# Kernel optimization log

Hardware: AMD Instinct MI355X
Metric: run time of the kernel (lower is better)

Reference implementation:

```python
import jax, jax.numpy as jnp
import numpy as np

B, SD, AD, H, QE, NQ = 16384, 512, 64, 1024, 64, 64


def setup_inputs() -> dict:
    key = jax.random.key(0)
    ks = jax.random.split(key, 12)
    s = 0.02
    p = lambda k, shape: (jax.random.normal(k, shape, jnp.float32) * s)
    return {
        "state": jax.random.normal(ks[0], (B, SD), jnp.float32),
        "action": jax.random.normal(ks[1], (B, AD), jnp.float32),
        # twin critics: leading axis 2 stacks q1 / q2 parameters
        "W_e1": p(ks[2], (2, QE, 1)),      "b_e1": p(ks[3], (2, QE)),
        "W_e2": p(ks[4], (2, QE, QE)),     "b_e2": p(ks[5], (2, QE)),
        "W_f1": p(ks[6], (2, H, SD + AD)), "b_f1": p(ks[7], (2, H)),
        "g1": jnp.ones((2, H), jnp.float32),  "beta1": jnp.zeros((2, H), jnp.float32),
        "W_f2": p(ks[8], (2, H, H)),       "b_f2": p(ks[9], (2, H)),
        "g2": jnp.ones((2, H), jnp.float32),  "beta2": jnp.zeros((2, H), jnp.float32),
        "W_h": p(ks[10], (2, 1, H + QE)),  "b_h": p(ks[11], (2, 1)),
    }


def _layernorm(x, g, b, eps=1e-5):
    mu = x.mean(-1, keepdims=True)
    var = ((x - mu) ** 2).mean(-1, keepdims=True)
    return (x - mu) * jax.lax.rsqrt(var + eps) * g + b


def _qnet(state, action, W_e1, b_e1, W_e2, b_e2, W_f1, b_f1, g1, beta1,
          W_f2, b_f2, g2, beta2, W_h, b_h):
    # feature_net (eval mode: dropout is identity)
    x = jnp.concatenate([state, action], axis=-1)            # [B, SD+AD]
    h = jax.nn.relu(_layernorm(x @ W_f1.T + b_f1, g1, beta1))
    feat = jax.nn.relu(_layernorm(h @ W_f2.T + b_f2, g2, beta2))  # [B, H]
    # tau embedding (batch-independent -> compute once per quantile, not per sample)
    tau = (jnp.linspace(0.0, 1.0, NQ + 1)[:-1] + 1.0 / (2 * NQ))[:, None]  # [NQ,1]
    te = jax.nn.relu(tau @ W_e1.T + b_e1) @ W_e2.T + b_e2    # [NQ, QE]
    # head on concat([feat, te]) == linear split (exact same math as the 64-iter loop)
    q_feat = feat @ W_h[0, :H]                               # [B]
    q_tau = te @ W_h[0, H:]                                  # [NQ]
    return q_feat[:, None] + q_tau[None, :] + b_h[0]         # [B, NQ]


def reference(state, action, W_e1, b_e1, W_e2, b_e2, W_f1, b_f1, g1, beta1,
              W_f2, b_f2, g2, beta2, W_h, b_h):
    qnet = lambda *ps: _qnet(state, action, *ps)
    q = jax.vmap(qnet)(W_e1, b_e1, W_e2, b_e2, W_f1, b_f1, g1, beta1,
                       W_f2, b_f2, g2, beta2, W_h, b_h)      # [2, B, NQ]
    return q[0], q[1]
```

## Files before the change

kernel.cpp:

```cpp
#include <hip/hip_runtime.h>
#include <stdint.h>

#define BATCH 16384
#define SDIM 512
#define ADIM 64
#define XDIM 576
#define HDIM 1024
#define NQD 64
#define QED 64

typedef __attribute__((ext_vector_type(8))) short short8;
typedef __attribute__((ext_vector_type(4))) float f32x4;

static __device__ inline unsigned short f2bf(float f) {
  unsigned int u = __float_as_uint(f);
  unsigned int r = (u + 0x7fffu + ((u >> 16) & 1u)) >> 16;
  return (unsigned short)r;
}
static __device__ inline float bf2f(unsigned short u) {
  return __uint_as_float(((unsigned int)u) << 16);
}

static __device__ inline void gload_lds16(const void* g, void* l) {
  __builtin_amdgcn_global_load_lds(
      (const __attribute__((address_space(1))) uint32_t*)g,
      (__attribute__((address_space(3))) uint32_t*)l, 16, 0, 0);
}

#define FENCE() asm volatile("" ::: "memory")


__global__ __launch_bounds__(256) void cvt_x(const float* __restrict__ st,
                                             const float* __restrict__ ac,
                                             unsigned short* __restrict__ xb) {
  const int total = BATCH * XDIM / 4;
  for (int i = blockIdx.x * blockDim.x + threadIdx.x; i < total;
       i += gridDim.x * blockDim.x) {
    const int e = i * 4;
    const int b = e / XDIM;
    const int j = e - b * XDIM;
    float4 v;
    if (j < SDIM) v = *(const float4*)(st + (size_t)b * SDIM + j);
    else          v = *(const float4*)(ac + (size_t)b * ADIM + (j - SDIM));
    ushort4 o;
    o.x = f2bf(v.x); o.y = f2bf(v.y); o.z = f2bf(v.z); o.w = f2bf(v.w);
    ((ushort4*)xb)[i] = o;
  }
}

__global__ __launch_bounds__(256) void cvt_w2(const float* __restrict__ s1,
                                              unsigned short* __restrict__ d1, int n1,
                                              const float* __restrict__ s2,
                                              unsigned short* __restrict__ d2, int n2) {
  for (int i = blockIdx.x * blockDim.x + threadIdx.x; i < n1 + n2;
       i += gridDim.x * blockDim.x) {
    const float4 v = (i < n1) ? ((const float4*)s1)[i] : ((const float4*)s2)[i - n1];
    ushort4 o;
    o.x = f2bf(v.x); o.y = f2bf(v.y); o.z = f2bf(v.z); o.w = f2bf(v.w);
    if (i < n1) ((ushort4*)d1)[i] = o; else ((ushort4*)d2)[i - n1] = o;
  }
}


__global__ void qtau_kernel(const float* __restrict__ We1, const float* __restrict__ be1,
                            const float* __restrict__ We2, const float* __restrict__ be2,
                            const float* __restrict__ Wh,  const float* __restrict__ bh,
                            float* __restrict__ qtau) {
  const int c = blockIdx.x >> 6;
  const int nq = blockIdx.x & 63;
  const int q = threadIdx.x;
  const float tau = (float)nq / 64.0f + 0.0078125f;
  float acc = be2[c * 64 + q];
  for (int e = 0; e < 64; ++e) {
    const float t1 = fmaxf(tau * We1[c * 64 + e] + be1[c * 64 + e], 0.0f);
    acc += t1 * We2[(c * 64 + q) * 64 + e];
  }
  float v = acc * Wh[c * (HDIM + QED) + HDIM + q];
  #pragma unroll
  for (int off = 32; off; off >>= 1) v += __shfl_xor(v, off);
  if (q == 0) qtau[c * 64 + nq] = v + bh[c];
}


template <int K>
__global__ __launch_bounds__(512, 2) void gemm_ring(const unsigned short* __restrict__ A,
                                                    const unsigned short* __restrict__ W,
                                                    const float* __restrict__ bias,
                                                    unsigned short* __restrict__ C) {
  constexpr int NT = K / 32;
  __shared__ unsigned short As[4][256][32];
  __shared__ unsigned short Bs[4][256][32];

  const int tid  = threadIdx.x;
  const int lane = tid & 63;
  const int wave = tid >> 6;
  const int wm = wave >> 2;
  const int wn = wave & 3;

  const int bid = (int)blockIdx.x;
  const int logical = (bid & 7) * 32 + (bid >> 3);
  const int mBase = (logical >> 2) * 256;
  const int nBase = (logical & 3) * 256;

  auto stage = [&](int ring, int kt) {
    #pragma unroll
    for (int i = 0; i < 2; ++i) {
      const int flat = i * 512 + tid;
      const int row  = flat >> 2;
      const int ps   = flat & 3;
      const int ls   = ps ^ ((row >> 1) & 3);
      gload_lds16(A + (size_t)(mBase + row) * K + kt * 32 + ls * 8,
                  &As[ring][0][0] + (size_t)flat * 8);
      gload_lds16(W + (size_t)(nBase + row) * K + kt * 32 + ls * 8,
                  &Bs[ring][0][0] + (size_t)flat * 8);
    }
  };

  f32x4 acc[8][4];
  #pragma unroll
  for (int fm = 0; fm < 8; ++fm)
    #pragma unroll
    for (int fn = 0; fn < 4; ++fn) {
      f32x4 z = {0.f, 0.f, 0.f, 0.f};
      acc[fm][fn] = z;
    }

  stage(0, 0);
  if (NT > 1) stage(1, 1);
  if (NT > 2) stage(2, 2);
  FENCE();
  if (NT > 2)      asm volatile("s_waitcnt vmcnt(8)" ::: "memory");
  else if (NT > 1) asm volatile("s_waitcnt vmcnt(4)" ::: "memory");
  else             asm volatile("s_waitcnt vmcnt(0)" ::: "memory");
  __builtin_amdgcn_s_barrier();
  FENCE();

  for (int t = 0; t < NT; ++t) {
    const int ring = t & 3;
    if (t + 3 < NT) stage((t + 3) & 3, t + 3);

    short8 af[8], bf[4];
    #pragma unroll
    for (int fm = 0; fm < 8; ++fm) {
      const int r  = wm * 128 + fm * 16 + (lane & 15);
      const int ps = (lane >> 4) ^ ((r >> 1) & 3);
      af[fm] = *(const short8*)&As[ring][r][ps * 8];
    }
    #pragma unroll
    for (int fn = 0; fn < 4; ++fn) {
      const int r  = wn * 64 + fn * 16 + (lane & 15);
      const int ps = (lane >> 4) ^ ((r >> 1) & 3);
      bf[fn] = *(const short8*)&Bs[ring][r][ps * 8];
    }

    __builtin_amdgcn_s_setprio(1);
    #pragma unroll
    for (int fm = 0; fm < 8; ++fm)
      #pragma unroll
      for (int fn = 0; fn < 4; ++fn)
        acc[fm][fn] = __builtin_amdgcn_mfma_f32_16x16x32_bf16(af[fm], bf[fn],
                                                              acc[fm][fn], 0, 0, 0);
    __builtin_amdgcn_s_setprio(0);

    if (t + 1 < NT) {
      FENCE();
      if (t + 3 < NT)      asm volatile("s_waitcnt vmcnt(8)" ::: "memory");
      else if (t + 2 < NT) asm volatile("s_waitcnt vmcnt(4)" ::: "memory");
      else                 asm volatile("s_waitcnt vmcnt(0)" ::: "memory");
      __builtin_amdgcn_s_barrier();
      FENCE();
    }
  }

  #pragma unroll
  for (int fm = 0; fm < 8; ++fm) {
    const int r0 = mBase + wm * 128 + fm * 16 + (lane >> 4) * 4;
    #pragma unroll
    for (int fn = 0; fn < 4; ++fn) {
      const int col = nBase + wn * 64 + fn * 16 + (lane & 15);
      const float bv = bias[col];
      #pragma unroll
      for (int j = 0; j < 4; ++j)
        C[(size_t)(r0 + j) * HDIM + col] = f2bf(acc[fm][fn][j] + bv);
    }
  }
}


template <bool HEAD>
__global__ __launch_bounds__(256) void ln_head(const unsigned short* __restrict__ X,
                                               const float* __restrict__ g,
                                               const float* __restrict__ bta,
                                               unsigned short* __restrict__ Y,
                                               const float* __restrict__ Wh,
                                               const float* __restrict__ qt,
                                               float* __restrict__ out) {
  const int b = blockIdx.x;
  const int tid = threadIdx.x;
  const int lane = tid & 63;
  const int wave = tid >> 6;
  __shared__ float rs_[4], rq_[4], rp_[4];

  const ushort4 xv = ((const ushort4*)(X + (size_t)b * HDIM))[tid];
  const float x0 = bf2f(xv.x), x1 = bf2f(xv.y), x2 = bf2f(xv.z), x3 = bf2f(xv.w);
  float s = x0 + x1 + x2 + x3;
  float q = x0 * x0 + x1 * x1 + x2 * x2 + x3 * x3;
  #pragma unroll
  for (int off = 32; off; off >>= 1) {
    s += __shfl_xor(s, off);
    q += __shfl_xor(q, off);
  }
  if (lane == 0) { rs_[wave] = s; rq_[wave] = q; }
  __syncthreads();
  s = rs_[0] + rs_[1] + rs_[2] + rs_[3];
  q = rq_[0] + rq_[1] + rq_[2] + rq_[3];
  const float mu = s * (1.0f / 1024.0f);
  const float var = q * (1.0f / 1024.0f) - mu * mu;
  const float rsig = rsqrtf(var + 1e-5f);

  const float4 gv = ((const float4*)g)[tid];
  const float4 bv = ((const float4*)bta)[tid];
  const float y0 = fmaxf((x0 - mu) * rsig * gv.x + bv.x, 0.0f);
  const float y1 = fmaxf((x1 - mu) * rsig * gv.y + bv.y, 0.0f);
  const float y2 = fmaxf((x2 - mu) * rsig * gv.z + bv.z, 0.0f);
  const float y3 = fmaxf((x3 - mu) * rsig * gv.w + bv.w, 0.0f);

  if constexpr (!HEAD) {
    ushort4 o;
    o.x = f2bf(y0); o.y = f2bf(y1); o.z = f2bf(y2); o.w = f2bf(y3);
    ((ushort4*)(Y + (size_t)b * HDIM))[tid] = o;
  } else {
    const float4 wv = ((const float4*)Wh)[tid];
    float p = y0 * wv.x + y1 * wv.y + y2 * wv.z + y3 * wv.w;
    #pragma unroll
    for (int off = 32; off; off >>= 1) p += __shfl_xor(p, off);
    if (lane == 0) rp_[wave] = p;
    __syncthreads();
    if (tid < 64) {
      const float qf = rp_[0] + rp_[1] + rp_[2] + rp_[3];
      out[(size_t)b * NQD + tid] = qf + qt[tid];
    }
  }
}


extern "C" void kernel_launch(void* const* d_in, const int* in_sizes, int n_in,
                              void* d_out, int out_size, void* d_ws, size_t ws_size,
                              hipStream_t stream) {
  (void)in_sizes; (void)n_in; (void)out_size; (void)ws_size;
  const float* state  = (const float*)d_in[0];
  const float* action = (const float*)d_in[1];
  const float* We1 = (const float*)d_in[2];
  const float* be1 = (const float*)d_in[3];
  const float* We2 = (const float*)d_in[4];
  const float* be2 = (const float*)d_in[5];
  const float* Wf1 = (const float*)d_in[6];
  const float* bW1 = (const float*)d_in[7];
  const float* g1  = (const float*)d_in[8];
  const float* bt1 = (const float*)d_in[9];
  const float* Wf2 = (const float*)d_in[10];
  const float* bW2 = (const float*)d_in[11];
  const float* g2  = (const float*)d_in[12];
  const float* bt2 = (const float*)d_in[13];
  const float* Wh  = (const float*)d_in[14];
  const float* bh  = (const float*)d_in[15];
  float* out = (float*)d_out;

  char* ws = (char*)d_ws;
  unsigned short* xb   = (unsigned short*)(ws);
  unsigned short* w1b  = (unsigned short*)(ws + 18874368);
  unsigned short* w2b  = (unsigned short*)(ws + 21233664);
  float*          qtw  = (float*)(ws + 25427968);
  unsigned short* ha   = (unsigned short*)(ws + 25428480);
  unsigned short* hb   = (unsigned short*)(ws + 58982912);

  cvt_x<<<2048, 256, 0, stream>>>(state, action, xb);
  cvt_w2<<<2048, 256, 0, stream>>>(Wf1, w1b, 2 * HDIM * XDIM / 4,
                                   Wf2, w2b, 2 * HDIM * HDIM / 4);
  qtau_kernel<<<128, 64, 0, stream>>>(We1, be1, We2, be2, Wh, bh, qtw);

  for (int c = 0; c < 2; ++c) {
    gemm_ring<XDIM><<<256, 512, 0, stream>>>(
        xb, w1b + (size_t)c * HDIM * XDIM, bW1 + c * HDIM, ha);
    ln_head<false><<<BATCH, 256, 0, stream>>>(
        ha, g1 + c * HDIM, bt1 + c * HDIM, hb, nullptr, nullptr, nullptr);
    gemm_ring<HDIM><<<256, 512, 0, stream>>>(
        hb, w2b + (size_t)c * HDIM * HDIM, bW2 + c * HDIM, ha);
    ln_head<true><<<BATCH, 256, 0, stream>>>(
        ha, g2 + c * HDIM, bt2 + c * HDIM, nullptr,
        Wh + (size_t)c * (HDIM + QED), qtw + c * 64, out + (size_t)c * BATCH * NQD);
  }
}
```

Baseline: 233.0 us.

## Shrink GEMM tiles to 256x128 with double buffering and merge conversion kernels

Result: faster. 213.5 us (-8.4%).

```diff
diff --git a/kernel.cpp b/kernel.cpp
--- a/kernel.cpp
+++ b/kernel.cpp
@@ -27,37 +27,37 @@
       (__attribute__((address_space(3))) uint32_t*)l, 16, 0, 0);
 }
 
-#define FENCE() asm volatile("" ::: "memory")
-
-
-__global__ __launch_bounds__(256) void cvt_x(const float* __restrict__ st,
-                                             const float* __restrict__ ac,
-                                             unsigned short* __restrict__ xb) {
-  const int total = BATCH * XDIM / 4;
-  for (int i = blockIdx.x * blockDim.x + threadIdx.x; i < total;
+
+__global__ __launch_bounds__(256) void prep(const float* __restrict__ st,
+                                            const float* __restrict__ ac,
+                                            unsigned short* __restrict__ xb,
+                                            const float* __restrict__ w1s,
+                                            unsigned short* __restrict__ w1d,
+                                            const float* __restrict__ w2s,
+                                            unsigned short* __restrict__ w2d) {
+  const int nx = BATCH * XDIM / 4;
+  const int n1 = 2 * HDIM * XDIM / 4;
+  const int n2 = 2 * HDIM * HDIM / 4;
+  for (int i = blockIdx.x * blockDim.x + threadIdx.x; i < nx + n1 + n2;
        i += gridDim.x * blockDim.x) {
-    const int e = i * 4;
-    const int b = e / XDIM;
-    const int j = e - b * XDIM;
     float4 v;
-    if (j < SDIM) v = *(const float4*)(st + (size_t)b * SDIM + j);
-    else          v = *(const float4*)(ac + (size_t)b * ADIM + (j - SDIM));
+    unsigned short* dst;
+    int di;
+    if (i < nx) {
+      const int e = i * 4;
+      const int b = e / XDIM;
+      const int j = e - b * XDIM;
+      if (j < SDIM) v = *(const float4*)(st + (size_t)b * SDIM + j);
+      else          v = *(const float4*)(ac + (size_t)b * ADIM + (j - SDIM));
+      dst = xb; di = i;
+    } else if (i < nx + n1) {
+      di = i - nx; v = ((const float4*)w1s)[di]; dst = w1d;
+    } else {
+      di = i - nx - n1; v = ((const float4*)w2s)[di]; dst = w2d;
+    }
     ushort4 o;
     o.x = f2bf(v.x); o.y = f2bf(v.y); o.z = f2bf(v.z); o.w = f2bf(v.w);
-    ((ushort4*)xb)[i] = o;
-  }
-}
-
-__global__ __launch_bounds__(256) void cvt_w2(const float* __restrict__ s1,
-                                              unsigned short* __restrict__ d1, int n1,
-                                              const float* __restrict__ s2,
-                                              unsigned short* __restrict__ d2, int n2) {
-  for (int i = blockIdx.x * blockDim.x + threadIdx.x; i < n1 + n2;
-       i += gridDim.x * blockDim.x) {
-    const float4 v = (i < n1) ? ((const float4*)s1)[i] : ((const float4*)s2)[i - n1];
-    ushort4 o;
-    o.x = f2bf(v.x); o.y = f2bf(v.y); o.z = f2bf(v.z); o.w = f2bf(v.w);
-    if (i < n1) ((ushort4*)d1)[i] = o; else ((ushort4*)d2)[i - n1] = o;
+    ((ushort4*)dst)[di] = o;
   }
 }
 
@@ -83,42 +83,45 @@
 
 
 template <int K>
-__global__ __launch_bounds__(512, 2) void gemm_ring(const unsigned short* __restrict__ A,
-                                                    const unsigned short* __restrict__ W,
-                                                    const float* __restrict__ bias,
-                                                    unsigned short* __restrict__ C) {
+__global__ __launch_bounds__(512, 4) void gemm_mn(const unsigned short* __restrict__ A,
+                                                  const unsigned short* __restrict__ W,
+                                                  const float* __restrict__ bias,
+                                                  unsigned short* __restrict__ C) {
   constexpr int NT = K / 32;
-  __shared__ unsigned short As[4][256][32];
-  __shared__ unsigned short Bs[4][256][32];
+  __shared__ unsigned short As[2][256][32];
+  __shared__ unsigned short Bs[2][128][32];
 
   const int tid  = threadIdx.x;
   const int lane = tid & 63;
   const int wave = tid >> 6;
-  const int wm = wave >> 2;
-  const int wn = wave & 3;
+  const int wm = wave >> 1;
+  const int wn = wave & 1;
 
   const int bid = (int)blockIdx.x;
-  const int logical = (bid & 7) * 32 + (bid >> 3);
-  const int mBase = (logical >> 2) * 256;
-  const int nBase = (logical & 3) * 256;
-
-  auto stage = [&](int ring, int kt) {
+  const int logical = (bid & 7) * 64 + (bid >> 3);
+  const int mBase = (logical >> 3) * 256;
+  const int nBase = (logical & 7) * 128;
+
+  auto stage = [&](int buf, int kt) {
     #pragma unroll
     for (int i = 0; i < 2; ++i) {
       const int flat = i * 512 + tid;
       const int row  = flat >> 2;
-      const int ps   = flat & 3;
-      const int ls   = ps ^ ((row >> 1) & 3);
+      const int ls   = (flat & 3) ^ ((row >> 1) & 3);
       gload_lds16(A + (size_t)(mBase + row) * K + kt * 32 + ls * 8,
-                  &As[ring][0][0] + (size_t)flat * 8);
+                  &As[buf][0][0] + (size_t)flat * 8);
+    }
+    {
+      const int row = tid >> 2;
+      const int ls  = (tid & 3) ^ ((row >> 1) & 3);
       gload_lds16(W + (size_t)(nBase + row) * K + kt * 32 + ls * 8,
-                  &Bs[ring][0][0] + (size_t)flat * 8);
+                  &Bs[buf][0][0] + (size_t)tid * 8);
     }
   };
 
-  f32x4 acc[8][4];
-  #pragma unroll
-  for (int fm = 0; fm < 8; ++fm)
+  f32x4 acc[4][4];
+  #pragma unroll
+  for (int fm = 0; fm < 4; ++fm)
     #pragma unroll
     for (int fn = 0; fn < 4; ++fn) {
       f32x4 z = {0.f, 0.f, 0.f, 0.f};
@@ -126,55 +129,40 @@
     }
 
   stage(0, 0);
-  if (NT > 1) stage(1, 1);
-  if (NT > 2) stage(2, 2);
-  FENCE();
-  if (NT > 2)      asm volatile("s_waitcnt vmcnt(8)" ::: "memory");
-  else if (NT > 1) asm volatile("s_waitcnt vmcnt(4)" ::: "memory");
-  else             asm volatile("s_waitcnt vmcnt(0)" ::: "memory");
-  __builtin_amdgcn_s_barrier();
-  FENCE();
+  __syncthreads();
 
   for (int t = 0; t < NT; ++t) {
-    const int ring = t & 3;
-    if (t + 3 < NT) stage((t + 3) & 3, t + 3);
-
-    short8 af[8], bf[4];
-    #pragma unroll
-    for (int fm = 0; fm < 8; ++fm) {
-      const int r  = wm * 128 + fm * 16 + (lane & 15);
+    const int buf = t & 1;
+    if (t + 1 < NT) stage(buf ^ 1, t + 1);
+
+    short8 af[4], bf[4];
+    #pragma unroll
+    for (int fm = 0; fm < 4; ++fm) {
+      const int r  = wm * 64 + fm * 16 + (lane & 15);
       const int ps = (lane >> 4) ^ ((r >> 1) & 3);
-      af[fm] = *(const short8*)&As[ring][r][ps * 8];
+      af[fm] = *(const short8*)&As[buf][r][ps * 8];
     }
     #pragma unroll
     for (int fn = 0; fn < 4; ++fn) {
       const int r  = wn * 64 + fn * 16 + (lane & 15);
       const int ps = (lane >> 4) ^ ((r >> 1) & 3);
-      bf[fn] = *(const short8*)&Bs[ring][r][ps * 8];
+      bf[fn] = *(const short8*)&Bs[buf][r][ps * 8];
     }
 
     __builtin_amdgcn_s_setprio(1);
     #pragma unroll
-    for (int fm = 0; fm < 8; ++fm)
+    for (int fm = 0; fm < 4; ++fm)
       #pragma unroll
       for (int fn = 0; fn < 4; ++fn)
         acc[fm][fn] = __builtin_amdgcn_mfma_f32_16x16x32_bf16(af[fm], bf[fn],
                                                               acc[fm][fn], 0, 0, 0);
     __builtin_amdgcn_s_setprio(0);
-
-    if (t + 1 < NT) {
-      FENCE();
-      if (t + 3 < NT)      asm volatile("s_waitcnt vmcnt(8)" ::: "memory");
-      else if (t + 2 < NT) asm volatile("s_waitcnt vmcnt(4)" ::: "memory");
-      else                 asm volatile("s_waitcnt vmcnt(0)" ::: "memory");
-      __builtin_amdgcn_s_barrier();
-      FENCE();
-    }
-  }
-
-  #pragma unroll
-  for (int fm = 0; fm < 8; ++fm) {
-    const int r0 = mBase + wm * 128 + fm * 16 + (lane >> 4) * 4;
+    __syncthreads();
+  }
+
+  #pragma unroll
+  for (int fm = 0; fm < 4; ++fm) {
+    const int r0 = mBase + wm * 64 + fm * 16 + (lane >> 4) * 4;
     #pragma unroll
     for (int fn = 0; fn < 4; ++fn) {
       const int col = nBase + wn * 64 + fn * 16 + (lane & 15);
@@ -274,17 +262,15 @@
   unsigned short* ha   = (unsigned short*)(ws + 25428480);
   unsigned short* hb   = (unsigned short*)(ws + 58982912);
 
-  cvt_x<<<2048, 256, 0, stream>>>(state, action, xb);
-  cvt_w2<<<2048, 256, 0, stream>>>(Wf1, w1b, 2 * HDIM * XDIM / 4,
-                                   Wf2, w2b, 2 * HDIM * HDIM / 4);
+  prep<<<2048, 256, 0, stream>>>(state, action, xb, Wf1, w1b, Wf2, w2b);
   qtau_kernel<<<128, 64, 0, stream>>>(We1, be1, We2, be2, Wh, bh, qtw);
 
   for (int c = 0; c < 2; ++c) {
-    gemm_ring<XDIM><<<256, 512, 0, stream>>>(
+    gemm_mn<XDIM><<<512, 512, 0, stream>>>(
         xb, w1b + (size_t)c * HDIM * XDIM, bW1 + c * HDIM, ha);
     ln_head<false><<<BATCH, 256, 0, stream>>>(
         ha, g1 + c * HDIM, bt1 + c * HDIM, hb, nullptr, nullptr, nullptr);
-    gemm_ring<HDIM><<<256, 512, 0, stream>>>(
+    gemm_mn<HDIM><<<512, 512, 0, stream>>>(
         hb, w2b + (size_t)c * HDIM * HDIM, bW2 + c * HDIM, ha);
     ln_head<true><<<BATCH, 256, 0, stream>>>(
         ha, g2 + c * HDIM, bt2 + c * HDIM, nullptr,
```
